# Optimization experiments

Measured on AMD Instinct MI355X. Metric: run time of the kernel, lower is better.

## Reference

```python
import jax, jax.numpy as jnp
import numpy as np

N_TOKENS = 100000
CUT = [0, 20000, 50000, 100000]  # cutoff_ends
D = 1024


def setup_inputs() -> dict:
    key = jax.random.key(0)
    ks = jax.random.split(key, 12)
    B, S = 2, 1024
    hidden = jax.random.normal(ks[0], (B, S, D), dtype=jnp.float32)
    target = jax.random.randint(ks[1], (B, S), 0, N_TOKENS, dtype=jnp.int64)
    s = 0.02
    # cluster 0 (shortlist) + cluster projection head
    w0 = jax.random.normal(ks[2], (20000, 1024), dtype=jnp.float32) * s
    b0 = jnp.zeros((20000,), jnp.float32)
    cluster_w = jax.random.normal(ks[3], (2, 1024), dtype=jnp.float32) * s  # n_clusters=2
    cluster_b = jnp.zeros((2,), jnp.float32)
    proj0 = jax.random.normal(ks[4], (1024, 1024), dtype=jnp.float32) * s  # d_proj x d_emb_0
    # tail cluster 1: d_emb_1 = 1024 // 4 = 256, vocab slice 20000..50000
    w1 = jax.random.normal(ks[5], (30000, 256), dtype=jnp.float32) * s
    b1 = jnp.zeros((30000,), jnp.float32)
    proj1 = jax.random.normal(ks[6], (1024, 256), dtype=jnp.float32) * s
    # tail cluster 2: d_emb_2 = 1024 // 16 = 64, vocab slice 50000..100000
    w2 = jax.random.normal(ks[7], (50000, 64), dtype=jnp.float32) * s
    b2 = jnp.zeros((50000,), jnp.float32)
    proj2 = jax.random.normal(ks[8], (1024, 64), dtype=jnp.float32) * s
    return {"hidden": hidden, "target": target,
            "w0": w0, "b0": b0, "cluster_w": cluster_w, "cluster_b": cluster_b, "proj0": proj0,
            "w1": w1, "b1": b1, "proj1": proj1,
            "w2": w2, "b2": b2, "proj2": proj2}


def reference(hidden, target, w0, b0, cluster_w, cluster_b, proj0,
              w1, b1, proj1, w2, b2, proj2):
    tgt_shape = target.shape
    h = hidden.reshape(-1, D)            # [N, d_proj]
    t = target.reshape(-1)               # [N]

    # head: shortlist logits + cluster logits, via low-rank projection
    head_w = jnp.concatenate([w0, cluster_w], axis=0)   # [20002, 1024]
    head_b = jnp.concatenate([b0, cluster_b], axis=0)
    head_logit = (h @ proj0) @ head_w.T + head_b        # [N, 20002]
    head_lp = jax.nn.log_softmax(head_logit, axis=1)

    nll = jnp.zeros(t.shape, h.dtype)

    # cluster 0 (shortlist): logprob is head_lp at the target id
    m0 = t < CUT[1]
    idx0 = jnp.clip(t, 0, CUT[1] - 1)
    lp0 = jnp.take_along_axis(head_lp, idx0[:, None], axis=1)[:, 0]
    nll = jnp.where(m0, -lp0, nll)

    # tail clusters. NOTE: faithful to original quirk head_logprob[:, -i]
    tails = [(CUT[1], CUT[2], w1, b1, proj1), (CUT[2], CUT[3], w2, b2, proj2)]
    for i, (left, right, w, b, p) in enumerate(tails, start=1):
        m = (t >= left) & (t < right)
        tail_logit = (h @ p) @ w.T + b                  # [N, right-left]
        tail_lp = jax.nn.log_softmax(tail_logit, axis=1)
        ti = jnp.clip(t - left, 0, right - left - 1)
        lp = head_lp[:, -i] + jnp.take_along_axis(tail_lp, ti[:, None], axis=1)[:, 0]
        nll = jnp.where(m, -lp, nll)

    return nll.reshape(tgt_shape)
```

## Files before the change

### kernel.cpp

```cpp
#include <hip/hip_runtime.h>
#include <cstdint>
#include <cstddef>

#define DEV static __device__ __forceinline__

typedef __attribute__((ext_vector_type(8))) short bf16x8_t;
typedef __attribute__((ext_vector_type(4))) float f32x4_t;

DEV unsigned short f2bf(float f) {
  union { float f; unsigned u; } v; v.f = f;
  unsigned r = v.u + 0x7fffu + ((v.u >> 16) & 1u);
  return (unsigned short)(r >> 16);
}

DEV void gl_lds16(const void* g, void* l) {
  __builtin_amdgcn_global_load_lds(
      (const __attribute__((address_space(1))) void*)g,
      (__attribute__((address_space(3))) void*)l,
      16, 0, 0);
}

__global__ __launch_bounds__(256)
void prep_k(const int* __restrict__ target,
            int* __restrict__ idx1, int* __restrict__ pos1,
            int* __restrict__ idx2, int* __restrict__ pos2,
            int* __restrict__ cnts,
            const float* __restrict__ p0, const float* __restrict__ p1,
            const float* __restrict__ p2, unsigned short* __restrict__ pAll,
            const float* __restrict__ s0, unsigned short* __restrict__ d0, int n0,
            const float* __restrict__ s1, unsigned short* __restrict__ d1, int n1,
            const float* __restrict__ s2, unsigned short* __restrict__ d2, int n2,
            const float* __restrict__ s3, unsigned short* __restrict__ d3, int n3,
            const float* __restrict__ s4, unsigned short* __restrict__ d4, int n4) {
  const int bid = blockIdx.x;
  const int tid = threadIdx.x;
  if (bid == 0) {
    __shared__ int c1, c2;
    if (tid == 0) { c1 = 0; c2 = 0; }
    __syncthreads();
    for (int i = tid; i < 2048; i += 256) {
      int t = target[i];
      if (t >= 20000 && t < 50000) {
        int p = atomicAdd(&c1, 1); idx1[p] = i; pos1[i] = p;
      } else if (t >= 50000) {
        int p = atomicAdd(&c2, 1); idx2[p] = i; pos2[i] = p;
      }
    }
    __syncthreads();
    if (tid == 0) { cnts[0] = c1; cnts[1] = c2; }
    return;
  }
  if (bid <= 1344) {
    __shared__ float tile[32][33];
    int b = bid - 1;
    const float* src; unsigned short* dst; int C, bx, by;
    if (b < 1024)      { src = p0; dst = pAll;               C = 1024; bx = b % 32; by = b / 32; }
    else if (b < 1280) { int q = b - 1024; src = p1; dst = pAll + 1024 * 1024; C = 256; bx = q % 8; by = q / 8; }
    else               { int q = b - 1280; src = p2; dst = pAll + 1280 * 1024; C = 64;  bx = q % 2; by = q / 2; }
    const int R = 1024;
    int tx = tid & 31, ty = tid >> 5;
    int c0 = bx * 32, r0 = by * 32;
    for (int yy = ty; yy < 32; yy += 8)
      tile[yy][tx] = src[(size_t)(r0 + yy) * C + (c0 + tx)];
    __syncthreads();
    for (int yy = ty; yy < 32; yy += 8)
      dst[(size_t)(c0 + yy) * R + (r0 + tx)] = f2bf(tile[tx][yy]);
    return;
  }
  int j = (bid - 1345) * 256 + tid;
  const float* s; unsigned short* d;
  if (j < n0) { s = s0; d = d0; }
  else { j -= n0;
    if (j < n1) { s = s1; d = d1; }
    else { j -= n1;
      if (j < n2) { s = s2; d = d2; }
      else { j -= n2;
        if (j < n3) { s = s3; d = d3; }
        else { j -= n3; if (j >= n4) return; s = s4; d = d4; }
      }
    }
  }
  float4 f = ((const float4*)s)[j];
  ushort4 o;
  o.x = f2bf(f.x); o.y = f2bf(f.y); o.z = f2bf(f.z); o.w = f2bf(f.w);
  ((ushort4*)d)[j] = o;
}

__global__ __launch_bounds__(256)
void proj_gemm_k(const unsigned short* __restrict__ A,
                 const unsigned short* __restrict__ W,
                 unsigned short* __restrict__ Cout) {
  __shared__ __align__(16) unsigned short As[128 * 32];
  __shared__ __align__(16) unsigned short Bs[128 * 32];
  const int K = 1024, V = 1344;
  const int tm = blockIdx.x, tn = blockIdx.y;
  const int m0 = tm * 128, n0 = tn * 128;
  const int tid = threadIdx.x, wid = tid >> 6, lane = tid & 63;
  const int quad = lane >> 4, l16 = lane & 15;
  const int wr = wid >> 1, wc = wid & 1;

  f32x4_t acc[4][4];
  const f32x4_t zero4 = {0.f, 0.f, 0.f, 0.f};
#pragma unroll
  for (int i = 0; i < 4; ++i)
#pragma unroll
    for (int j = 0; j < 4; ++j) acc[i][j] = zero4;

  const int srow = wid * 32 + (lane >> 2);
  const int skk  = (lane & 3) * 8;
  const unsigned short* Ap0 = A + (size_t)(m0 + srow) * K + skk;
  const unsigned short* Ap1 = A + (size_t)(m0 + srow + 16) * K + skk;
  int wrow0 = n0 + srow;      if (wrow0 > V - 1) wrow0 = V - 1;
  int wrow1 = n0 + srow + 16; if (wrow1 > V - 1) wrow1 = V - 1;
  const unsigned short* Wp0 = W + (size_t)wrow0 * K + skk;
  const unsigned short* Wp1 = W + (size_t)wrow1 * K + skk;
  unsigned short* Asw = As + wid * 1024;
  unsigned short* Bsw = Bs + wid * 1024;

  for (int k0 = 0; k0 < K; k0 += 32) {
    gl_lds16(Ap0, Asw);
    gl_lds16(Ap1, Asw + 512);
    gl_lds16(Wp0, Bsw);
    gl_lds16(Wp1, Bsw + 512);
    Ap0 += 32; Ap1 += 32; Wp0 += 32; Wp1 += 32;
    __syncthreads();
    bf16x8_t af[4], bfr[4];
#pragma unroll
    for (int i = 0; i < 4; ++i)
      af[i] = *(const bf16x8_t*)(As + (size_t)(wr * 64 + i * 16 + l16) * 32 + quad * 8);
#pragma unroll
    for (int j = 0; j < 4; ++j)
      bfr[j] = *(const bf16x8_t*)(Bs + (size_t)(wc * 64 + j * 16 + l16) * 32 + quad * 8);
#pragma unroll
    for (int i = 0; i < 4; ++i)
#pragma unroll
      for (int j = 0; j < 4; ++j)
        acc[i][j] = __builtin_amdgcn_mfma_f32_16x16x32_bf16(af[i], bfr[j], acc[i][j], 0, 0, 0);
    __syncthreads();
  }
#pragma unroll
  for (int i = 0; i < 4; ++i)
#pragma unroll
    for (int j = 0; j < 4; ++j) {
      const int n = n0 + wc * 64 + j * 16 + l16;
      if (n < V) {
#pragma unroll
        for (int r = 0; r < 4; ++r) {
          const int m = m0 + wr * 64 + i * 16 + quad * 4 + r;
          Cout[(size_t)m * V + n] = f2bf(acc[i][j][r]);
        }
      }
    }
}

__global__ __launch_bounds__(256)
void head_k(const unsigned short* __restrict__ Pall,
            const unsigned short* __restrict__ w0b,
            const float* __restrict__ b0, const float* __restrict__ cb,
            float* __restrict__ part0, float* __restrict__ g0,
            float* __restrict__ cg, const int* __restrict__ target) {
  __shared__ __align__(16) unsigned short As[128 * 32];
  __shared__ __align__(16) unsigned short Bs[128 * 32];
  __shared__ float red[2][128];

  const int bid = blockIdx.x;
  const int x = (bid >> 3) & 15;
  const int y = ((bid >> 7) << 3) | (bid & 7);
  if (y >= 157) return;
  const int K = 1024, V = 20002, Vmain = 20000, ldA = 1344;
  const int m0 = x * 128, n0 = y * 128;

  const int tid = threadIdx.x, wid = tid >> 6, lane = tid & 63;
  const int quad = lane >> 4, l16 = lane & 15;
  const int wr = wid >> 1, wc = wid & 1;

  f32x4_t acc[4][4];
  const f32x4_t zero4 = {0.f, 0.f, 0.f, 0.f};
#pragma unroll
  for (int i = 0; i < 4; ++i)
#pragma unroll
    for (int j = 0; j < 4; ++j) acc[i][j] = zero4;

  const int srow = wid * 32 + (lane >> 2);
  const int skk  = (lane & 3) * 8;
  const unsigned short* Ap0 = Pall + (size_t)(m0 + srow) * ldA + skk;
  const unsigned short* Ap1 = Pall + (size_t)(m0 + srow + 16) * ldA + skk;
  int wrow0 = n0 + srow;      if (wrow0 > V - 1) wrow0 = V - 1;
  int wrow1 = n0 + srow + 16; if (wrow1 > V - 1) wrow1 = V - 1;
  const unsigned short* Wp0 = w0b + (size_t)wrow0 * K + skk;
  const unsigned short* Wp1 = w0b + (size_t)wrow1 * K + skk;
  unsigned short* Asw = As + wid * 1024;
  unsigned short* Bsw = Bs + wid * 1024;

  for (int k0 = 0; k0 < K; k0 += 32) {
    gl_lds16(Ap0, Asw);
    gl_lds16(Ap1, Asw + 512);
    gl_lds16(Wp0, Bsw);
    gl_lds16(Wp1, Bsw + 512);
    Ap0 += 32; Ap1 += 32; Wp0 += 32; Wp1 += 32;
    __syncthreads();
    bf16x8_t af[4], bfr[4];
#pragma unroll
    for (int i = 0; i < 4; ++i)
      af[i] = *(const bf16x8_t*)(As + (size_t)(wr * 64 + i * 16 + l16) * 32 + quad * 8);
#pragma unroll
    for (int j = 0; j < 4; ++j)
      bfr[j] = *(const bf16x8_t*)(Bs + (size_t)(wc * 64 + j * 16 + l16) * 32 + quad * 8);
#pragma unroll
    for (int i = 0; i < 4; ++i)
#pragma unroll
      for (int j = 0; j < 4; ++j)
        acc[i][j] = __builtin_amdgcn_mfma_f32_16x16x32_bf16(af[i], bfr[j], acc[i][j], 0, 0, 0);
    __syncthreads();
  }

  int nj[4]; float bj[4];
#pragma unroll
  for (int j = 0; j < 4; ++j) {
    nj[j] = n0 + wc * 64 + j * 16 + l16;
    bj[j] = (nj[j] < Vmain) ? b0[nj[j]] : ((nj[j] < V) ? cb[nj[j] - Vmain] : 0.f);
  }
#pragma unroll
  for (int i = 0; i < 4; ++i) {
#pragma unroll
    for (int r = 0; r < 4; ++r) {
      const int row = wr * 64 + i * 16 + quad * 4 + r;
      const int token = m0 + row;
      float v[4], sum = 0.f;
#pragma unroll
      for (int j = 0; j < 4; ++j) {
        v[j] = acc[i][j][r] + bj[j];
        if (nj[j] < V) sum += __expf(v[j]);
      }
#pragma unroll
      for (int off = 1; off < 16; off <<= 1)
        sum += __shfl_xor(sum, off, 64);
      if (l16 == 0) red[wc][row] = sum;
      const int t = target[token];
      const int gi = (t < 19999) ? t : 19999;
#pragma unroll
      for (int j = 0; j < 4; ++j) {
        if (nj[j] == gi) g0[token] = v[j];
        if (nj[j] == 20000) cg[2 * token]     = v[j];
        if (nj[j] == 20001) cg[2 * token + 1] = v[j];
      }
    }
  }
  __syncthreads();
  if (tid < 128)
    part0[(size_t)(m0 + tid) * 157 + y] = red[0][tid] + red[1][tid];
}

template <int KT>
__global__ __launch_bounds__(256, 1)
void tail_stripe_k(const unsigned short* __restrict__ A, int ldA,
                   const unsigned short* __restrict__ W,
                   const float* __restrict__ bias, int V, int ntiles,
                   const int* __restrict__ rowidx,
                   const int* __restrict__ cnt_ptr,
                   float* __restrict__ partials,
                   float* __restrict__ gathered,
                   const int* __restrict__ target, int glo) {
  constexpr int NC = KT / 32;
  __shared__ __align__(16) unsigned short Ws[NC][128 * 32];
  __shared__ __align__(16) unsigned short As[NC][128 * 32];
  __shared__ float red[2][128];

  const int tn = blockIdx.x, n0 = tn * 128;
  const int Meff = *cnt_ptr;
  const int tid = threadIdx.x, wid = tid >> 6, lane = tid & 63;
  const int quad = lane >> 4, l16 = lane & 15;
  const int wr = wid >> 1, wc = wid & 1;
  const int srow = wid * 32 + (lane >> 2);
  const int skk  = (lane & 3) * 8;

  int wrow0 = n0 + srow;      if (wrow0 > V - 1) wrow0 = V - 1;
  int wrow1 = n0 + srow + 16; if (wrow1 > V - 1) wrow1 = V - 1;
#pragma unroll
  for (int c = 0; c < NC; ++c) {
    gl_lds16(W + (size_t)wrow0 * KT + c * 32 + skk, Ws[c] + wid * 1024);
    gl_lds16(W + (size_t)wrow1 * KT + c * 32 + skk, Ws[c] + wid * 1024 + 512);
  }

  int nj[4]; float bj[4];
#pragma unroll
  for (int j = 0; j < 4; ++j) {
    nj[j] = n0 + wc * 64 + j * 16 + l16;
    bj[j] = (nj[j] < V) ? bias[nj[j]] : 0.f;
  }

  const int nm = (Meff + 127) >> 7;
  for (int m = 0; m < nm; ++m) {
    const int m0 = m * 128;
    int ar0 = m0 + srow;      if (ar0 > Meff - 1) ar0 = Meff - 1;
    int ar1 = m0 + srow + 16; if (ar1 > Meff - 1) ar1 = Meff - 1;
    ar0 = rowidx[ar0]; ar1 = rowidx[ar1];
#pragma unroll
    for (int c = 0; c < NC; ++c) {
      gl_lds16(A + (size_t)ar0 * ldA + c * 32 + skk, As[c] + wid * 1024);
      gl_lds16(A + (size_t)ar1 * ldA + c * 32 + skk, As[c] + wid * 1024 + 512);
    }
    __syncthreads();

    f32x4_t acc[4][4];
    const f32x4_t zero4 = {0.f, 0.f, 0.f, 0.f};
#pragma unroll
    for (int i = 0; i < 4; ++i)
#pragma unroll
      for (int j = 0; j < 4; ++j) acc[i][j] = zero4;
#pragma unroll
    for (int c = 0; c < NC; ++c) {
      bf16x8_t af[4], bfr[4];
#pragma unroll
      for (int i = 0; i < 4; ++i)
        af[i] = *(const bf16x8_t*)(As[c] + (size_t)(wr * 64 + i * 16 + l16) * 32 + quad * 8);
#pragma unroll
      for (int j = 0; j < 4; ++j)
        bfr[j] = *(const bf16x8_t*)(Ws[c] + (size_t)(wc * 64 + j * 16 + l16) * 32 + quad * 8);
#pragma unroll
      for (int i = 0; i < 4; ++i)
#pragma unroll
        for (int j = 0; j < 4; ++j)
          acc[i][j] = __builtin_amdgcn_mfma_f32_16x16x32_bf16(af[i], bfr[j], acc[i][j], 0, 0, 0);
    }

#pragma unroll
    for (int i = 0; i < 4; ++i) {
#pragma unroll
      for (int r = 0; r < 4; ++r) {
        const int row = wr * 64 + i * 16 + quad * 4 + r;
        const int gr = m0 + row;
        const int grc = (gr < Meff) ? gr : (Meff - 1);
        const int token = rowidx[grc];
        float v[4], sum = 0.f;
#pragma unroll
        for (int j = 0; j < 4; ++j) {
          v[j] = acc[i][j][r] + bj[j];
          if (nj[j] < V) sum += __expf(v[j]);
        }
#pragma unroll
        for (int off = 1; off < 16; off <<= 1)
          sum += __shfl_xor(sum, off, 64);
        if (l16 == 0) red[wc][row] = sum;
        const int gi = target[token] - glo;
#pragma unroll
        for (int j = 0; j < 4; ++j)
          if (nj[j] == gi) gathered[token] = v[j];
      }
    }
    __syncthreads();
    if (tid < 128 && (m0 + tid) < Meff)
      partials[(size_t)(m0 + tid) * ntiles + tn] = red[0][tid] + red[1][tid];
  }
}

__global__ __launch_bounds__(256)
void combine_k(const float* __restrict__ part0,
               const float* __restrict__ part1, int nt1,
               const float* __restrict__ part2, int nt2,
               const float* __restrict__ g0, const float* __restrict__ g1,
               const float* __restrict__ g2, const float* __restrict__ cg,
               const int* __restrict__ pos1, const int* __restrict__ pos2,
               const int* __restrict__ target, float* __restrict__ out) {
  const int w = threadIdx.x >> 6, lane = threadIdx.x & 63;
  const int token = blockIdx.x * 4 + w;
  const int t = target[token];

  float S = 0.f;
  for (int i = lane; i < 157; i += 64)
    S += part0[(size_t)token * 157 + i];
#pragma unroll
  for (int off = 1; off < 64; off <<= 1)
    S += __shfl_xor(S, off, 64);
  const float lse_head = __logf(S);

  float res;
  if (t < 20000) {
    res = lse_head - g0[token];
  } else {
    const float* pt; int nt; float gv, ch; int row;
    if (t < 50000) { pt = part1; nt = nt1; gv = g1[token]; ch = cg[2 * token + 1]; row = pos1[token]; }
    else           { pt = part2; nt = nt2; gv = g2[token]; ch = cg[2 * token];     row = pos2[token]; }
    float S2 = 0.f;
    for (int i = lane; i < nt; i += 64)
      S2 += pt[(size_t)row * nt + i];
#pragma unroll
    for (int off = 1; off < 64; off <<= 1)
      S2 += __shfl_xor(S2, off, 64);
    float lse_t = __logf(S2);
    res = -((ch - lse_head) + (gv - lse_t));
  }
  if (lane == 0) out[token] = res;
}

extern "C" void kernel_launch(void* const* d_in, const int* in_sizes, int n_in,
                              void* d_out, int out_size, void* d_ws, size_t ws_size,
                              hipStream_t stream) {
  (void)in_sizes; (void)n_in; (void)out_size; (void)ws_size;
  const float* hidden = (const float*)d_in[0];
  const int*   target = (const int*)d_in[1];
  const float* w0     = (const float*)d_in[2];
  const float* b0     = (const float*)d_in[3];
  const float* cw     = (const float*)d_in[4];
  const float* cb     = (const float*)d_in[5];
  const float* proj0  = (const float*)d_in[6];
  const float* w1     = (const float*)d_in[7];
  const float* b1     = (const float*)d_in[8];
  const float* proj1  = (const float*)d_in[9];
  const float* w2     = (const float*)d_in[10];
  const float* b2     = (const float*)d_in[11];
  const float* proj2  = (const float*)d_in[12];
  float* out = (float*)d_out;

  const int NT1 = 235, NT2 = 391;

  char* p = (char*)d_ws;
  auto alloc = [&](size_t bytes) {
    char* r = p; p += (bytes + 255) & ~(size_t)255; return r;
  };
  unsigned short* Hb   = (unsigned short*)alloc(2048ull * 1024 * 2);
  unsigned short* pAll = (unsigned short*)alloc(1344ull * 1024 * 2);
  unsigned short* w0b  = (unsigned short*)alloc(20002ull * 1024 * 2);
  unsigned short* w1b  = (unsigned short*)alloc(30000ull * 256 * 2);
  unsigned short* w2b  = (unsigned short*)alloc(50000ull * 64 * 2);
  unsigned short* Pall = (unsigned short*)alloc(2048ull * 1344 * 2);
  float* part0 = (float*)alloc(2048ull * 157 * 4);
  float* part1 = (float*)alloc(2048ull * NT1 * 4);
  float* part2 = (float*)alloc(2048ull * NT2 * 4);
  float* g0 = (float*)alloc(2048 * 4);
  float* g1 = (float*)alloc(2048 * 4);
  float* g2 = (float*)alloc(2048 * 4);
  float* cg = (float*)alloc(2048 * 2 * 4);
  int* idx1 = (int*)alloc(2048 * 4);
  int* pos1 = (int*)alloc(2048 * 4);
  int* idx2 = (int*)alloc(2048 * 4);
  int* pos2 = (int*)alloc(2048 * 4);
  int* cnts = (int*)alloc(2 * 4);

  const int c_h = 2048 * 1024 / 4, c_w0 = 20000 * 1024 / 4, c_cw = 2048 / 4,
            c_w1 = 30000 * 256 / 4, c_w2 = 50000 * 64 / 4;
  const int ctot = c_h + c_w0 + c_cw + c_w1 + c_w2;
  const int nb_cast = (ctot + 255) / 256;
  prep_k<<<1 + 1344 + nb_cast, 256, 0, stream>>>(
      target, idx1, pos1, idx2, pos2, cnts,
      proj0, proj1, proj2, pAll,
      hidden, Hb, c_h,
      w0, w0b, c_w0,
      cw, w0b + 20000ull * 1024, c_cw,
      w1, w1b, c_w1,
      w2, w2b, c_w2);

  proj_gemm_k<<<dim3(16, 11), 256, 0, stream>>>(Hb, pAll, Pall);

  head_k<<<2560, 256, 0, stream>>>(Pall, w0b, b0, cb, part0, g0, cg, target);

  tail_stripe_k<256><<<NT1, 256, 0, stream>>>(
      Pall + 1024, 1344, w1b, b1, 30000, NT1, idx1, cnts + 0,
      part1, g1, target, 20000);
  tail_stripe_k<64><<<NT2, 256, 0, stream>>>(
      Pall + 1280, 1344, w2b, b2, 50000, NT2, idx2, cnts + 1,
      part2, g2, target, 50000);

  combine_k<<<512, 256, 0, stream>>>(part0, part1, NT1, part2, NT2,
      g0, g1, g2, cg, pos1, pos2, target, out);
}
```

Baseline: 428.3 us.

## Rewrite head GEMM as 256x256 tile with double-buffered, swizzled LDS pipeline

Replaces the 128x128 head GEMM with a 512-thread, 256x256-tile kernel using K-tiles of 64. LDS is double-buffered, loads are issued asynchronously and interleaved with MFMA phases under explicit barriers, priority hints and a swizzled LDS layout. Partial softmax sums per token drop from 157 to 79 stripes, and the combine kernel is updated to match. This aims to raise data reuse and hide memory latency in the dominant head GEMM. The cost is heavier register pressure and fragile hand-scheduled waitcnt logic.

```diff
diff --git a/kernel.cpp b/kernel.cpp
--- a/kernel.cpp
+++ b/kernel.cpp
@@ -153,79 +153,177 @@
     }
 }
 
-__global__ __launch_bounds__(256)
-void head_k(const unsigned short* __restrict__ Pall,
-            const unsigned short* __restrict__ w0b,
-            const float* __restrict__ b0, const float* __restrict__ cb,
-            float* __restrict__ part0, float* __restrict__ g0,
-            float* __restrict__ cg, const int* __restrict__ target) {
-  __shared__ __align__(16) unsigned short As[128 * 32];
-  __shared__ __align__(16) unsigned short Bs[128 * 32];
-  __shared__ float red[2][128];
-
+
+#define SBAR()                                                                \
+  __builtin_amdgcn_sched_barrier(0);                                          \
+  __builtin_amdgcn_s_barrier();                                               \
+  __builtin_amdgcn_sched_barrier(0)
+
+#define LGKM0()                                                               \
+  asm volatile("s_waitcnt lgkmcnt(0)" ::: "memory");                          \
+  __builtin_amdgcn_sched_barrier(0)
+
+#define STA(BUF, HALF, KT)                                                    \
+  {                                                                           \
+    const unsigned short* g_ = aB0 + (size_t)(HALF) * (128 * 1344) + (KT) * 64; \
+    char* d_ = (char*)SA[BUF][HALF] + ldsw;                                   \
+    gl_lds16(g_, d_);                                                         \
+    gl_lds16(g_ + 64 * 1344, d_ + 8192);                                      \
+  }
+
+#define STB(BUF, HALF, KT)                                                    \
+  {                                                                           \
+    char* d_ = (char*)SB[BUF][HALF] + ldsw;                                   \
+    gl_lds16(bP##HALF##0 + (KT) * 64, d_);                                    \
+    gl_lds16(bP##HALF##1 + (KT) * 64, d_ + 8192);                             \
+  }
+
+#define MM16(mb, nb)                                                          \
+  {                                                                           \
+    _Pragma("unroll") for (int mi = 0; mi < 4; ++mi) {                        \
+      _Pragma("unroll") for (int nj = 0; nj < 2; ++nj) {                      \
+        acc[(mb) + mi][(nb) + nj] = __builtin_amdgcn_mfma_f32_16x16x32_bf16(  \
+            Af[0][mi], Bf[(nb) / 2][0][nj], acc[(mb) + mi][(nb) + nj], 0, 0, 0); \
+        acc[(mb) + mi][(nb) + nj] = __builtin_amdgcn_mfma_f32_16x16x32_bf16(  \
+            Af[1][mi], Bf[(nb) / 2][1][nj], acc[(mb) + mi][(nb) + nj], 0, 0, 0); \
+      }                                                                       \
+    }                                                                         \
+  }
+
+#define PH(D_, E_, KTV)                                                       \
+  {                                                                           \
+    const int kt_ = (KTV);                                                    \
+    const int t1_ = (kt_ + 1 > 15) ? 15 : (kt_ + 1);                          \
+    const int t2_ = (kt_ + 2 > 15) ? 15 : (kt_ + 2);                          \
+                             \
+    _Pragma("unroll") for (int kk = 0; kk < 2; ++kk) {                        \
+      _Pragma("unroll") for (int mi = 0; mi < 4; ++mi)                        \
+          Af[kk][mi] = *(const bf16x8_t*)(pa##D_ + mi * 2048 + kk * 64);      \
+      _Pragma("unroll") for (int nj = 0; nj < 2; ++nj)                        \
+          Bf[0][kk][nj] = *(const bf16x8_t*)(pb##D_ + nj * 2048 + kk * 64);   \
+    }                                                                         \
+    STB(E_, 1, t1_);                                                          \
+    SBAR();                                                                   \
+    LGKM0();                                                                  \
+    __builtin_amdgcn_s_setprio(1);                                            \
+    MM16(0, 0);                                                               \
+    __builtin_amdgcn_s_setprio(0);                                            \
+    SBAR();                                                                   \
+                                     \
+    _Pragma("unroll") for (int kk = 0; kk < 2; ++kk) {                        \
+      _Pragma("unroll") for (int nj = 0; nj < 2; ++nj)                        \
+          Bf[1][kk][nj] = *(const bf16x8_t*)(pb##D_ + (2 + nj) * 2048 + kk * 64); \
+    }                                                                         \
+    STA(E_, 1, t1_);                                                          \
+    SBAR();                                                                   \
+    LGKM0();                                                                  \
+    __builtin_amdgcn_s_setprio(1);                                            \
+    MM16(0, 2);                                                               \
+    __builtin_amdgcn_s_setprio(0);                                            \
+    SBAR();                                                                   \
+                                     \
+    _Pragma("unroll") for (int kk = 0; kk < 2; ++kk) {                        \
+      _Pragma("unroll") for (int mi = 0; mi < 4; ++mi)                        \
+          Af[kk][mi] = *(const bf16x8_t*)(pa##D_ + (4 + mi) * 2048 + kk * 64); \
+    }                                                                         \
+    STB(D_, 0, t2_);                                                          \
+    SBAR();                                                                   \
+    LGKM0();                                                                  \
+    __builtin_amdgcn_s_setprio(1);                                            \
+    MM16(4, 0);                                                               \
+    __builtin_amdgcn_s_setprio(0);                                            \
+    SBAR();                                                                   \
+                    \
+    STA(D_, 0, t2_);                                                          \
+    SBAR();                                                                   \
+    __builtin_amdgcn_s_setprio(1);                                            \
+    MM16(4, 2);                                                               \
+    __builtin_amdgcn_s_setprio(0);                                            \
+    asm volatile("s_waitcnt vmcnt(4)" ::: "memory");                          \
+    SBAR();                                                                   \
+  }
+
+__global__ __launch_bounds__(512, 2)
+void head256_k(const unsigned short* __restrict__ Pall,
+               const unsigned short* __restrict__ w0b,
+               const float* __restrict__ b0, const float* __restrict__ cb,
+               float* __restrict__ part0, float* __restrict__ g0,
+               float* __restrict__ cg, const int* __restrict__ target) {
+  __shared__ __align__(16) unsigned short SA[2][2][8192];
+  __shared__ __align__(16) unsigned short SB[2][2][8192];
+
+  const int V = 20002;
   const int bid = blockIdx.x;
-  const int x = (bid >> 3) & 15;
-  const int y = ((bid >> 7) << 3) | (bid & 7);
-  if (y >= 157) return;
-  const int K = 1024, V = 20002, Vmain = 20000, ldA = 1344;
-  const int m0 = x * 128, n0 = y * 128;
-
-  const int tid = threadIdx.x, wid = tid >> 6, lane = tid & 63;
+  const int orig = (bid & 7) * 79 + (bid >> 3);
+  const int mt = orig & 7, stripe = orig >> 3;
+  const int m0 = mt * 256, n0 = stripe * 256;
+
+  const int tid = threadIdx.x;
+  const int wid = tid >> 6, lane = tid & 63;
   const int quad = lane >> 4, l16 = lane & 15;
-  const int wr = wid >> 1, wc = wid & 1;
-
-  f32x4_t acc[4][4];
+  const int wr = wid >> 2, wc = wid & 3;
+
+  const int P0v = tid * 16;
+  const int Ls = P0v ^ (((P0v >> 9) & 1) << 5);
+  const int r0 = Ls >> 7;
+  const int ibh = (Ls & 127) >> 1;
+
+  const unsigned short* aB0 = Pall + (size_t)(m0 + r0) * 1344 + ibh;
+  int br00 = n0 + r0;            if (br00 > V - 1) br00 = V - 1;
+  int br01 = n0 + r0 + 64;       if (br01 > V - 1) br01 = V - 1;
+  int br10 = n0 + 128 + r0;      if (br10 > V - 1) br10 = V - 1;
+  int br11 = n0 + 128 + r0 + 64; if (br11 > V - 1) br11 = V - 1;
+  const unsigned short* bP00 = w0b + (size_t)br00 * 1024 + ibh;
+  const unsigned short* bP01 = w0b + (size_t)br01 * 1024 + ibh;
+  const unsigned short* bP10 = w0b + (size_t)br10 * 1024 + ibh;
+  const unsigned short* bP11 = w0b + (size_t)br11 * 1024 + ibh;
+
+  const int ldsw = wid * 1024;
+
+  const int aoff = (l16 * 128 + quad * 16) ^ (((l16 >> 2) & 1) << 5);
+  const char* pa0 = (const char*)SA[0][wr] + aoff;
+  const char* pa1 = (const char*)SA[1][wr] + aoff;
+  const char* pb0 = (const char*)SB[0][wc >> 1] + (wc & 1) * 8192 + aoff;
+  const char* pb1 = (const char*)SB[1][wc >> 1] + (wc & 1) * 8192 + aoff;
+
+  f32x4_t acc[8][4];
   const f32x4_t zero4 = {0.f, 0.f, 0.f, 0.f};
 #pragma unroll
-  for (int i = 0; i < 4; ++i)
+  for (int i = 0; i < 8; ++i)
 #pragma unroll
     for (int j = 0; j < 4; ++j) acc[i][j] = zero4;
 
-  const int srow = wid * 32 + (lane >> 2);
-  const int skk  = (lane & 3) * 8;
-  const unsigned short* Ap0 = Pall + (size_t)(m0 + srow) * ldA + skk;
-  const unsigned short* Ap1 = Pall + (size_t)(m0 + srow + 16) * ldA + skk;
-  int wrow0 = n0 + srow;      if (wrow0 > V - 1) wrow0 = V - 1;
-  int wrow1 = n0 + srow + 16; if (wrow1 > V - 1) wrow1 = V - 1;
-  const unsigned short* Wp0 = w0b + (size_t)wrow0 * K + skk;
-  const unsigned short* Wp1 = w0b + (size_t)wrow1 * K + skk;
-  unsigned short* Asw = As + wid * 1024;
-  unsigned short* Bsw = Bs + wid * 1024;
-
-  for (int k0 = 0; k0 < K; k0 += 32) {
-    gl_lds16(Ap0, Asw);
-    gl_lds16(Ap1, Asw + 512);
-    gl_lds16(Wp0, Bsw);
-    gl_lds16(Wp1, Bsw + 512);
-    Ap0 += 32; Ap1 += 32; Wp0 += 32; Wp1 += 32;
-    __syncthreads();
-    bf16x8_t af[4], bfr[4];
-#pragma unroll
-    for (int i = 0; i < 4; ++i)
-      af[i] = *(const bf16x8_t*)(As + (size_t)(wr * 64 + i * 16 + l16) * 32 + quad * 8);
-#pragma unroll
-    for (int j = 0; j < 4; ++j)
-      bfr[j] = *(const bf16x8_t*)(Bs + (size_t)(wc * 64 + j * 16 + l16) * 32 + quad * 8);
-#pragma unroll
-    for (int i = 0; i < 4; ++i)
-#pragma unroll
-      for (int j = 0; j < 4; ++j)
-        acc[i][j] = __builtin_amdgcn_mfma_f32_16x16x32_bf16(af[i], bfr[j], acc[i][j], 0, 0, 0);
-    __syncthreads();
-  }
+  bf16x8_t Af[2][4];
+  bf16x8_t Bf[2][2][2];
+
+  STB(0, 0, 0); STA(0, 0, 0); STB(0, 1, 0); STA(0, 1, 0);
+  STB(1, 0, 1); STA(1, 0, 1);
+  asm volatile("s_waitcnt vmcnt(4)" ::: "memory");
+  SBAR();
+
+#pragma unroll 1
+  for (int ktp = 0; ktp < 8; ++ktp) {
+    const int kt0 = 2 * ktp;
+    PH(0, 1, kt0);
+    PH(1, 0, kt0 + 1);
+  }
+
+  asm volatile("s_waitcnt vmcnt(0)" ::: "memory");
+  SBAR();
 
   int nj[4]; float bj[4];
 #pragma unroll
   for (int j = 0; j < 4; ++j) {
     nj[j] = n0 + wc * 64 + j * 16 + l16;
-    bj[j] = (nj[j] < Vmain) ? b0[nj[j]] : ((nj[j] < V) ? cb[nj[j] - Vmain] : 0.f);
-  }
-#pragma unroll
-  for (int i = 0; i < 4; ++i) {
+    bj[j] = (nj[j] < 20000) ? b0[nj[j]] : ((nj[j] < V) ? cb[nj[j] - 20000] : 0.f);
+  }
+  float* redf = (float*)&SA[0][0][0];
+#pragma unroll
+  for (int i = 0; i < 8; ++i) {
 #pragma unroll
     for (int r = 0; r < 4; ++r) {
-      const int row = wr * 64 + i * 16 + quad * 4 + r;
-      const int token = m0 + row;
+      const int rloc = i * 16 + quad * 4 + r;
+      const int token = m0 + wr * 128 + rloc;
       float v[4], sum = 0.f;
 #pragma unroll
       for (int j = 0; j < 4; ++j) {
@@ -235,7 +333,7 @@
 #pragma unroll
       for (int off = 1; off < 16; off <<= 1)
         sum += __shfl_xor(sum, off, 64);
-      if (l16 == 0) red[wc][row] = sum;
+      if (l16 == 0) redf[(wr * 4 + wc) * 128 + rloc] = sum;
       const int t = target[token];
       const int gi = (t < 19999) ? t : 19999;
 #pragma unroll
@@ -247,9 +345,20 @@
     }
   }
   __syncthreads();
-  if (tid < 128)
-    part0[(size_t)(m0 + tid) * 157 + y] = red[0][tid] + red[1][tid];
-}
+  if (tid < 256) {
+    const int wrr = tid >> 7, rr = tid & 127;
+    const float s = redf[(wrr * 4 + 0) * 128 + rr] + redf[(wrr * 4 + 1) * 128 + rr]
+                  + redf[(wrr * 4 + 2) * 128 + rr] + redf[(wrr * 4 + 3) * 128 + rr];
+    part0[(size_t)(m0 + tid) * 79 + stripe] = s;
+  }
+}
+
+#undef PH
+#undef MM16
+#undef STA
+#undef STB
+#undef SBAR
+#undef LGKM0
 
 template <int KT>
 __global__ __launch_bounds__(256, 1)
@@ -367,8 +476,8 @@
   const int t = target[token];
 
   float S = 0.f;
-  for (int i = lane; i < 157; i += 64)
-    S += part0[(size_t)token * 157 + i];
+  for (int i = lane; i < 79; i += 64)
+    S += part0[(size_t)token * 79 + i];
 #pragma unroll
   for (int off = 1; off < 64; off <<= 1)
     S += __shfl_xor(S, off, 64);
@@ -424,7 +533,7 @@
   unsigned short* w1b  = (unsigned short*)alloc(30000ull * 256 * 2);
   unsigned short* w2b  = (unsigned short*)alloc(50000ull * 64 * 2);
   unsigned short* Pall = (unsigned short*)alloc(2048ull * 1344 * 2);
-  float* part0 = (float*)alloc(2048ull * 157 * 4);
+  float* part0 = (float*)alloc(2048ull * 79 * 4);
   float* part1 = (float*)alloc(2048ull * NT1 * 4);
   float* part2 = (float*)alloc(2048ull * NT2 * 4);
   float* g0 = (float*)alloc(2048 * 4);
@@ -452,7 +561,7 @@
 
   proj_gemm_k<<<dim3(16, 11), 256, 0, stream>>>(Hb, pAll, Pall);
 
-  head_k<<<2560, 256, 0, stream>>>(Pall, w0b, b0, cb, part0, g0, cg, target);
+  head256_k<<<632, 512, 0, stream>>>(Pall, w0b, b0, cb, part0, g0, cg, target);
 
   tail_stripe_k<256><<<NT1, 256, 0, stream>>>(
       Pall + 1024, 1344, w1b, b1, 30000, NT1, idx1, cnts + 0,
```

Result: slower. 444.8 us (+3.8%).
